# Kernel tuning notes

Hardware: AMD Instinct MI355X
Metric: run time of the kernel (lower is better)

The kernel has to match this reference:

```python
import jax, jax.numpy as jnp
import numpy as np

N_TYPES = 4  # global / and / or / leaf node types (indep_weights)


def gcn_layer(x, W_stack, b, edge_src, edge_dst, edge_w, labels, num_nodes):
    # Per-node-type dense projection: compute all 4 projections, then select by label.
    # all4: [4, N, out]
    all4 = jnp.einsum('nd,kdo->kno', x, W_stack)
    support = jnp.take_along_axis(all4, labels[None, :, None].astype(jnp.int32), axis=0)[0]  # [N, out]
    # Sparse adjacency propagation: out[dst] += w * support[src]  (torch.spmm equivalent)
    msgs = support[edge_src] * edge_w[:, None]  # [E, out]
    agg = jax.ops.segment_sum(msgs, edge_dst, num_segments=num_nodes)
    return agg + b


def setup_inputs() -> dict:
    key = jax.random.key(0)
    ks = jax.random.split(key, 12)
    N, E = 50000, 1600000
    nfeat, nhid, nclass = 256, 256, 64
    x = jax.random.normal(ks[0], (N, nfeat), dtype=jnp.float32)
    edge_src = jax.random.randint(ks[1], (E,), 0, N, dtype=jnp.int32)
    edge_dst = jax.random.randint(ks[2], (E,), 0, N, dtype=jnp.int32)
    edge_w = jax.random.uniform(ks[3], (E,), dtype=jnp.float32)
    labels = jax.random.randint(ks[4], (N,), 0, N_TYPES, dtype=jnp.int32)
    def winit(k, fi, fo):
        s = 1.0 / np.sqrt(fo)
        return jax.random.uniform(k, (N_TYPES, fi, fo), minval=-s, maxval=s, dtype=jnp.float32)
    def binit(k, fo):
        s = 1.0 / np.sqrt(fo)
        return jax.random.uniform(k, (fo,), minval=-s, maxval=s, dtype=jnp.float32)
    return {
        'x': x, 'edge_src': edge_src, 'edge_dst': edge_dst, 'edge_w': edge_w, 'labels': labels,
        'W1': winit(ks[5], nfeat, nhid), 'b1': binit(ks[6], nhid),
        'W2': winit(ks[7], nhid, nhid), 'b2': binit(ks[8], nhid),
        'W3': winit(ks[9], nhid, nclass), 'b3': binit(ks[10], nclass),
    }


def reference(x, edge_src, edge_dst, edge_w, labels, W1, b1, W2, b2, W3, b3):
    N = x.shape[0]
    h = jax.nn.relu(gcn_layer(x, W1, b1, edge_src, edge_dst, edge_w, labels, N))
    # F.dropout with p=0 (module default) is identity
    h = jax.nn.relu(gcn_layer(h, W2, b2, edge_src, edge_dst, edge_w, labels, N))
    out = gcn_layer(h, W3, b3, edge_src, edge_dst, edge_w, labels, N)
    return out
```

## Files before the change

### kernel.cpp

```cpp
#include <hip/hip_runtime.h>
#include <hip/hip_bf16.h>

#define NT 4
#define FEAT 256
#define OUT3 64

typedef __bf16 bf16x8 __attribute__((ext_vector_type(8)));
typedef float  f32x4  __attribute__((ext_vector_type(4)));

__device__ inline unsigned int f2bf_bits(float f) {
    __hip_bfloat16 h = __float2bfloat16(f);
    unsigned short u;
    __builtin_memcpy(&u, &h, 2);
    return (unsigned int)u;
}
__device__ inline float bfl(unsigned int u) { return __uint_as_float(u << 16); }
__device__ inline float bfh(unsigned int u) { return __uint_as_float(u & 0xffff0000u); }
__device__ __host__ inline int nat_of(int p) {
    int lo = p & 63;
    return (p & ~63) | (((lo & 3) << 4) | (lo >> 2));
}

__global__ __launch_bounds__(512) void pass_a(const int* __restrict__ dst,
                                              const int* __restrict__ labels,
                                              int* __restrict__ bcnt, int* __restrict__ lc,
                                              int E, int N) {
    __shared__ int h[256];
    __shared__ int lh[NT];
    int tid = threadIdx.x;
    if (tid < 256) h[tid] = 0;
    if (tid < NT) lh[tid] = 0;
    __syncthreads();
    int base = blockIdx.x * 4096;
#pragma unroll
    for (int k = 0; k < 8; ++k) {
        int e = base + k * 512 + tid;
        if (e < E) atomicAdd(&h[((unsigned)dst[e]) >> 8], 1);
    }
#pragma unroll
    for (int k = 0; k < 8; ++k) {
        int i = base + k * 512 + tid;
        if (i < N) atomicAdd(&lh[labels[i]], 1);
    }
    __syncthreads();
    if (tid < 256) { int v = h[tid]; if (v) atomicAdd(&bcnt[tid], v); }
    if (tid < NT) { int v = lh[tid]; if (v) atomicAdd(&lc[tid], v); }
}

__global__ __launch_bounds__(256) void scan_master(
    const int* __restrict__ bcnt, const int* __restrict__ lc,
    int* __restrict__ boff, int* __restrict__ gcur, int* __restrict__ rowoff,
    int* __restrict__ lstart, int NB, int N, int E) {
    __shared__ int s[256];
    int tid = threadIdx.x;
    int own = (tid < NB) ? bcnt[tid] : 0;
    s[tid] = own;
    __syncthreads();
    for (int d = 1; d < 256; d <<= 1) {
        int v = (tid >= d) ? s[tid - d] : 0;
        __syncthreads();
        s[tid] += v;
        __syncthreads();
    }
    int excl = s[tid] - own;
    if (tid < NB) { boff[tid] = excl; gcur[tid] = excl; }
    if (tid == 0) {
        boff[NB] = E; rowoff[N] = E;
        int run = 0;
        for (int l = 0; l < NT; ++l) {
            lstart[l] = run;
            run += (lc[l] + 63) & ~63;
        }
    }
}

__global__ void scatter_nodes(const int* __restrict__ labels, const int* __restrict__ lstart,
                              int* __restrict__ lcur, int* __restrict__ iperm, int N) {
    int n = blockIdx.x * 256 + threadIdx.x;
    int lab = (n < N) ? labels[n] : -1;
    int lane = threadIdx.x & 63;
    for (int l = 0; l < NT; ++l) {
        unsigned long long m = __ballot(lab == l);
        if (m == 0ull) continue;
        int leader = __builtin_ctzll(m);
        int base = 0;
        if (lane == leader) base = atomicAdd(&lcur[l], (int)__popcll(m));
        base = __shfl(base, leader, 64);
        if (lab == l) {
            int prefix = (int)__popcll(m & ((1ull << lane) - 1ull));
            iperm[n] = lstart[l] + base + prefix;
        }
    }
}

__global__ __launch_bounds__(512) void fuse_a(
    const int* __restrict__ src, const int* __restrict__ dst, const float* __restrict__ w,
    const int* __restrict__ iperm, int* __restrict__ gcur, uint2* __restrict__ earr, int E,
    const float* __restrict__ x, unsigned short* __restrict__ actLo,
    unsigned short* __restrict__ actHi, int total4,
    const float* __restrict__ W1, const float* __restrict__ W2, const float* __restrict__ W3,
    const float* __restrict__ b1, const float* __restrict__ b2,
    unsigned short* __restrict__ W1b, unsigned short* __restrict__ W2b,
    unsigned short* __restrict__ W3b, float* __restrict__ biasPerm,
    int nbEB, int nbX) {
    int tid = threadIdx.x;
    int blk = (int)blockIdx.x;
    if (blk < nbEB) {
        __shared__ int h[256];
        __shared__ int basearr[256];
        if (tid < 256) h[tid] = 0;
        __syncthreads();
        int base = blk * 4096;
        int b[8], rank[8], px[8]; float wv[8];
#pragma unroll
        for (int k = 0; k < 8; ++k) {
            int e = base + k * 512 + tid;
            if (e < E) {
                int d = dst[e];
                b[k] = ((unsigned)d) >> 8;
                px[k] = iperm[src[e]] | ((d & 255) << 16);
                wv[k] = w[e];
                rank[k] = atomicAdd(&h[b[k]], 1);
            } else b[k] = -1;
        }
        __syncthreads();
        if (tid < 256) { int c = h[tid]; basearr[tid] = c ? atomicAdd(&gcur[tid], c) : 0; }
        __syncthreads();
#pragma unroll
        for (int k = 0; k < 8; ++k) {
            if (b[k] >= 0) {
                int pos = basearr[b[k]] + rank[k];
                earr[pos] = make_uint2((unsigned)px[k], __float_as_uint(wv[k]));
            }
        }
    } else if (blk < nbEB + nbX) {
        int i = (blk - nbEB) * 512 + tid;
        if (i < total4) {
            float4 v = ((const float4*)x)[i];
            unsigned int lo = f2bf_bits(v.x) | (f2bf_bits(v.y) << 16);
            unsigned int hi = f2bf_bits(v.z) | (f2bf_bits(v.w) << 16);
            int slot = iperm[i >> 6];
            unsigned short* dp = ((i & 63) >= 32) ? actHi : actLo;
            ((uint2*)dp)[(size_t)slot * 32 + (i & 31)] = make_uint2(lo, hi);
        }
    } else {
        const int S = NT * FEAT * FEAT;
        const int S3 = NT * FEAT * OUT3;
        int idx = (blk - nbEB - nbX) * 512 + tid;
        if (idx < 2 * S + S3) {
            const float* W; unsigned short* D; int OUTF; int t; bool remap;
            if (idx < S)          { W = W1; D = W1b; OUTF = FEAT; t = idx;         remap = false; }
            else if (idx < 2 * S) { W = W2; D = W2b; OUTF = FEAT; t = idx - S;     remap = true; }
            else                  { W = W3; D = W3b; OUTF = OUT3; t = idx - 2 * S; remap = true; }
            int n = t % OUTF;
            int r = t / OUTF;
            int j = r & 7, q = (r >> 3) & 3, k0 = (r >> 5) & 7, lab = r >> 8;
            int k_slot = k0 * 32 + q * 8 + j;
            int k_src = remap ? nat_of(k_slot) : k_slot;
            float f = W[((size_t)(lab * FEAT + k_src)) * OUTF + n];
            D[(((size_t)lab * 8 + k0) * OUTF + n) * 32 + q * 8 + j] = (unsigned short)f2bf_bits(f);
        } else {
            int p2 = idx - (2 * S + S3);
            if (p2 < 256) biasPerm[p2] = b1[nat_of(p2)];
            else if (p2 < 512) biasPerm[p2] = b2[nat_of(p2 - 256)];
        }
    }
}

__device__ void bucket_sort_body(int b, const uint2* __restrict__ earr,
                                 const int* __restrict__ boff, int* __restrict__ rowoff,
                                 unsigned int* __restrict__ edata, int N) {
    int s = boff[b], e = boff[b + 1];
    __shared__ int cnt[256], off[256];
    int tid = threadIdx.x;
    cnt[tid] = 0;
    __syncthreads();
    for (int i = s + tid; i < e; i += 256) atomicAdd(&cnt[(earr[i].x >> 16) & 255], 1);
    __syncthreads();
    off[tid] = cnt[tid];
    __syncthreads();
    for (int d = 1; d < 256; d <<= 1) {
        int v = (tid >= d) ? off[tid - d] : 0;
        __syncthreads();
        off[tid] += v;
        __syncthreads();
    }
    int excl = off[tid] - cnt[tid];
    int node = b * 256 + tid;
    if (node < N) rowoff[node] = s + excl;
    off[tid] = excl;
    __syncthreads();
    for (int i = s + tid; i < e; i += 256) {
        uint2 r = earr[i];
        int d = (r.x >> 16) & 255;
        int k = atomicAdd(&off[d], 1);
        edata[s + k] = (f2bf_bits(__uint_as_float(r.y)) << 16) | (r.x & 0xffff);
    }
}

__device__ void proj256_body(int gb,
                             const unsigned short* __restrict__ actLo,
                             const unsigned short* __restrict__ actHi,
                             const unsigned short* __restrict__ Wswz,
                             const int* __restrict__ lstart,
                             unsigned short* __restrict__ supLo,
                             unsigned short* __restrict__ supHi) {
    int warp = threadIdx.x >> 6;
    int lane = threadIdx.x & 63;
    int m0 = gb * 64;
    int lab = (m0 >= lstart[1]) + (m0 >= lstart[2]) + (m0 >= lstart[3]);
    int q = lane >> 4, c = lane & 15;
    int n0 = warp * 64;

    const unsigned short* aLo = actLo + (size_t)(m0 + c) * 128 + q * 8;
    const unsigned short* aHi = actHi + (size_t)(m0 + c) * 128 + q * 8;
    const unsigned short* bb = Wswz + (size_t)lab * FEAT * 256 + (size_t)(n0 + c) * 32 + q * 8;

    f32x4 acc[4][4] = {};
#pragma unroll
    for (int k0 = 0; k0 < 8; ++k0) {
        const unsigned short* abase = (k0 < 4) ? aLo : aHi;
        int koff = (k0 & 3) * 32;
        bf16x8 a[4];
#pragma unroll
        for (int t = 0; t < 4; ++t) a[t] = *(const bf16x8*)(abase + (size_t)t * 2048 + koff);
        const unsigned short* bk = bb + (size_t)k0 * 32 * 256;
#pragma unroll
        for (int u = 0; u < 4; ++u) {
            bf16x8 bfrag = *(const bf16x8*)(bk + u * 512);
#pragma unroll
            for (int t = 0; t < 4; ++t)
                acc[t][u] = __builtin_amdgcn_mfma_f32_16x16x32_bf16(a[t], bfrag, acc[t][u], 0, 0, 0);
        }
    }
    uint2* ov = (uint2*)((n0 >= 128) ? supHi : supLo);
    int cix = ((n0 & 64) >> 2) + c;
#pragma unroll
    for (int t = 0; t < 4; ++t) {
#pragma unroll
        for (int r = 0; r < 4; ++r) {
            int row = m0 + t * 16 + q * 4 + r;
            unsigned int lo = f2bf_bits(acc[t][0][r]) | (f2bf_bits(acc[t][1][r]) << 16);
            unsigned int hi = f2bf_bits(acc[t][2][r]) | (f2bf_bits(acc[t][3][r]) << 16);
            ov[(size_t)row * 32 + cix] = make_uint2(lo, hi);
        }
    }
}

__global__ __launch_bounds__(256) void fuse_b(
    const uint2* __restrict__ earr, const int* __restrict__ boff,
    int* __restrict__ rowoff, unsigned int* __restrict__ edata, int N, int NB,
    const unsigned short* __restrict__ actLo, const unsigned short* __restrict__ actHi,
    const unsigned short* __restrict__ Wswz, const int* __restrict__ lstart,
    unsigned short* __restrict__ supLo, unsigned short* __restrict__ supHi) {
    int blk = (int)blockIdx.x;
    if (blk < NB) bucket_sort_body(blk, earr, boff, rowoff, edata, N);
    else proj256_body(blk - NB, actLo, actHi, Wswz, lstart, supLo, supHi);
}

__global__ __launch_bounds__(256) void proj256_kernel(
    const unsigned short* __restrict__ actLo, const unsigned short* __restrict__ actHi,
    const unsigned short* __restrict__ Wswz, const int* __restrict__ lstart,
    unsigned short* __restrict__ supLo, unsigned short* __restrict__ supHi) {
    proj256_body((int)blockIdx.x, actLo, actHi, Wswz, lstart, supLo, supHi);
}

__global__ __launch_bounds__(256) void proj64_kernel(
    const unsigned short* __restrict__ actLo, const unsigned short* __restrict__ actHi,
    const unsigned short* __restrict__ Wswz, const int* __restrict__ lstart,
    unsigned short* __restrict__ outp) {
    int warp = threadIdx.x >> 6;
    int lane = threadIdx.x & 63;
    int m0 = blockIdx.x * 64;
    int lab = (m0 >= lstart[1]) + (m0 >= lstart[2]) + (m0 >= lstart[3]);
    int q = lane >> 4, c = lane & 15;
    int mb = m0 + warp * 16;

    const unsigned short* aLo = actLo + (size_t)(mb + c) * 128 + q * 8;
    const unsigned short* aHi = actHi + (size_t)(mb + c) * 128 + q * 8;
    const unsigned short* bb = Wswz + (size_t)lab * FEAT * OUT3 + (size_t)c * 32 + q * 8;

    f32x4 acc[4] = {};
#pragma unroll
    for (int k0 = 0; k0 < 8; ++k0) {
        const unsigned short* abase = (k0 < 4) ? aLo : aHi;
        bf16x8 a = *(const bf16x8*)(abase + (k0 & 3) * 32);
        const unsigned short* bk = bb + (size_t)k0 * 32 * OUT3;
#pragma unroll
        for (int u = 0; u < 4; ++u) {
            bf16x8 bfrag = *(const bf16x8*)(bk + u * 512);
            acc[u] = __builtin_amdgcn_mfma_f32_16x16x32_bf16(a, bfrag, acc[u], 0, 0, 0);
        }
    }
    uint2* ov = (uint2*)outp;
#pragma unroll
    for (int r = 0; r < 4; ++r) {
        int row = mb + q * 4 + r;
        unsigned int lo = f2bf_bits(acc[0][r]) | (f2bf_bits(acc[1][r]) << 16);
        unsigned int hi = f2bf_bits(acc[2][r]) | (f2bf_bits(acc[3][r]) << 16);
        ov[(size_t)row * 16 + c] = make_uint2(lo, hi);
    }
}

__global__ __launch_bounds__(256) void agg256h_kernel(
    const unsigned int* __restrict__ sup, const int* __restrict__ rowoff,
    const unsigned int* __restrict__ edata, const int* __restrict__ iperm,
    const float* __restrict__ biasHalf, unsigned int* __restrict__ outp, int N) {
    int warp = __builtin_amdgcn_readfirstlane((int)(threadIdx.x >> 6));
    int node = (int)blockIdx.x * 4 + warp;
    if (node >= N) return;
    int lane = threadIdx.x & 63;
    int s = __builtin_amdgcn_readfirstlane(rowoff[node]);
    int e = __builtin_amdgcn_readfirstlane(rowoff[node + 1]);
    int slot = __builtin_amdgcn_readfirstlane(iperm[node]);
    float a0 = 0.f, a1 = 0.f;
    int j = s;
    for (; j + 16 <= e; j += 16) {
        unsigned int ed[16], v[16];
#pragma unroll
        for (int u = 0; u < 16; ++u) ed[u] = edata[j + u];
#pragma unroll
        for (int u = 0; u < 16; ++u) v[u] = sup[(size_t)(ed[u] & 0xffff) * 64 + lane];
#pragma unroll
        for (int u = 0; u < 16; ++u) {
            float w = __uint_as_float(ed[u] & 0xffff0000u);
            a0 += w * bfl(v[u]); a1 += w * bfh(v[u]);
        }
    }
    if (j < e) {
        unsigned int ed[16], v[16]; float wm[16];
#pragma unroll
        for (int u = 0; u < 16; ++u) {
            int jj = j + u;
            int jc = (jj < e) ? jj : e - 1;
            ed[u] = edata[jc];
            wm[u] = (jj < e) ? __uint_as_float(ed[u] & 0xffff0000u) : 0.f;
        }
#pragma unroll
        for (int u = 0; u < 16; ++u) v[u] = sup[(size_t)(ed[u] & 0xffff) * 64 + lane];
#pragma unroll
        for (int u = 0; u < 16; ++u) { a0 += wm[u] * bfl(v[u]); a1 += wm[u] * bfh(v[u]); }
    }
    float2 b = ((const float2*)biasHalf)[lane];
    a0 = fmaxf(a0 + b.x, 0.f);
    a1 = fmaxf(a1 + b.y, 0.f);
    outp[(size_t)slot * 64 + lane] = f2bf_bits(a0) | (f2bf_bits(a1) << 16);
}

__global__ __launch_bounds__(256) void agg64_kernel(
    const unsigned short* __restrict__ sup, const int* __restrict__ rowoff,
    const unsigned int* __restrict__ edata, const float* __restrict__ b3,
    float* __restrict__ outp, int N) {
    int warp = __builtin_amdgcn_readfirstlane((int)(threadIdx.x >> 6));
    int node = (int)blockIdx.x * 4 + warp;
    if (node >= N) return;
    int lane = threadIdx.x & 63;
    int s = __builtin_amdgcn_readfirstlane(rowoff[node]);
    int e = __builtin_amdgcn_readfirstlane(rowoff[node + 1]);
    float a = 0.f;
    int j = s;
    for (; j + 8 <= e; j += 8) {
        unsigned int ed[8]; unsigned short v[8];
#pragma unroll
        for (int u = 0; u < 8; ++u) ed[u] = edata[j + u];
#pragma unroll
        for (int u = 0; u < 8; ++u) v[u] = sup[(size_t)(ed[u] & 0xffff) * 64 + lane];
#pragma unroll
        for (int u = 0; u < 8; ++u)
            a += __uint_as_float(ed[u] & 0xffff0000u) * __uint_as_float((unsigned int)v[u] << 16);
    }
    if (j < e) {
        unsigned int ed[8]; float wm[8]; unsigned short v[8];
#pragma unroll
        for (int u = 0; u < 8; ++u) {
            int jj = j + u;
            int jc = (jj < e) ? jj : e - 1;
            ed[u] = edata[jc];
            wm[u] = (jj < e) ? __uint_as_float(ed[u] & 0xffff0000u) : 0.f;
        }
#pragma unroll
        for (int u = 0; u < 8; ++u) v[u] = sup[(size_t)(ed[u] & 0xffff) * 64 + lane];
#pragma unroll
        for (int u = 0; u < 8; ++u)
            a += wm[u] * __uint_as_float((unsigned int)v[u] << 16);
    }
    int natp = (((lane & 3) << 4) | (lane >> 2));
    outp[(size_t)node * 64 + natp] = a + b3[natp];
}

extern "C" void kernel_launch(void* const* d_in, const int* in_sizes, int n_in,
                              void* d_out, int out_size, void* d_ws, size_t ws_size,
                              hipStream_t stream) {
    const float* x        = (const float*)d_in[0];
    const int*   edge_src = (const int*)d_in[1];
    const int*   edge_dst = (const int*)d_in[2];
    const float* edge_w   = (const float*)d_in[3];
    const int*   labels   = (const int*)d_in[4];
    const float* W1 = (const float*)d_in[5];
    const float* b1 = (const float*)d_in[6];
    const float* W2 = (const float*)d_in[7];
    const float* b2 = (const float*)d_in[8];
    const float* W3 = (const float*)d_in[9];
    const float* b3 = (const float*)d_in[10];

    const int N = in_sizes[0] / FEAT;
    const int E = in_sizes[1];
    const int NB = (N + 255) >> 8;
    const int G64 = (N + NT * 64 + 63) / 64;
    const int slotCap = G64 * 64;

    char* p = (char*)d_ws;
    auto alloc = [&](size_t bytes) -> char* {
        char* r = p;
        p += (bytes + 255) & ~(size_t)255;
        return r;
    };
    unsigned short* bufA = (unsigned short*)alloc((size_t)slotCap * FEAT * 2);
    unsigned short* bufB = (unsigned short*)alloc((size_t)slotCap * FEAT * 2);
    unsigned short* W1b  = (unsigned short*)alloc((size_t)NT * FEAT * FEAT * 2);
    unsigned short* W2b  = (unsigned short*)alloc((size_t)NT * FEAT * FEAT * 2);
    unsigned short* W3b  = (unsigned short*)alloc((size_t)NT * FEAT * OUT3 * 2);
    float*        biasPerm = (float*)alloc(512 * 4);
    int*          rowoff = (int*)alloc((size_t)(N + 1) * 4);
    unsigned int* edata  = (unsigned int*)alloc((size_t)E * 4);
    int*          iperm  = (int*)alloc((size_t)N * 4);
    int*          counters = (int*)alloc(264 * 4);
    int*          boff   = (int*)alloc(257 * 4);
    int*          gcur   = (int*)alloc(256 * 4);
    int*          lstart = (int*)alloc(64);
    int* bcnt = counters;
    int* lc   = counters + 256;
    int* lcur = counters + 260;

    unsigned short* actLo = bufA;
    unsigned short* actHi = bufA + (size_t)slotCap * 128;
    unsigned short* supLo = bufB;
    unsigned short* supHi = bufB + (size_t)slotCap * 128;
    uint2* earr = (uint2*)d_out;

    const int nbEB = (E + 4095) / 4096;
    const int total4 = N * 64;
    const int nbX = (total4 + 511) / 512;
    const int totW = 2 * NT * FEAT * FEAT + NT * FEAT * OUT3 + 512;
    const int nbW = (totW + 511) / 512;

    hipMemsetAsync(counters, 0, 264 * 4, stream);
    pass_a<<<nbEB, 512, 0, stream>>>(edge_dst, labels, bcnt, lc, E, N);
    scan_master<<<1, 256, 0, stream>>>(bcnt, lc, boff, gcur, rowoff, lstart, NB, N, E);
    scatter_nodes<<<(N + 255) / 256, 256, 0, stream>>>(labels, lstart, lcur, iperm, N);
    fuse_a<<<nbEB + nbX + nbW, 512, 0, stream>>>(
        edge_src, edge_dst, edge_w, iperm, gcur, earr, E,
        x, actLo, actHi, total4,
        W1, W2, W3, b1, b2, W1b, W2b, W3b, biasPerm, nbEB, nbX);

    const int aggGrid = (N + 3) / 4;
    fuse_b<<<NB + G64, 256, 0, stream>>>(earr, boff, rowoff, edata, N, NB,
                                         actLo, actHi, W1b, lstart, supLo, supHi);
    agg256h_kernel<<<aggGrid, 256, 0, stream>>>((const unsigned int*)supLo, rowoff, edata, iperm,
                                                biasPerm + 0, (unsigned int*)actLo, N);
    agg256h_kernel<<<aggGrid, 256, 0, stream>>>((const unsigned int*)supHi, rowoff, edata, iperm,
                                                biasPerm + 128, (unsigned int*)actHi, N);
    proj256_kernel<<<G64, 256, 0, stream>>>(actLo, actHi, W2b, lstart, supLo, supHi);
    agg256h_kernel<<<aggGrid, 256, 0, stream>>>((const unsigned int*)supLo, rowoff, edata, iperm,
                                                biasPerm + 256, (unsigned int*)actLo, N);
    agg256h_kernel<<<aggGrid, 256, 0, stream>>>((const unsigned int*)supHi, rowoff, edata, iperm,
                                                biasPerm + 384, (unsigned int*)actHi, N);
    proj64_kernel<<<G64, 256, 0, stream>>>(actLo, actHi, W3b, lstart, bufB);
    agg64_kernel<<<aggGrid, 256, 0, stream>>>(bufB, rowoff, edata, b3, (float*)d_out, N);
}
```

Baseline: 481.2 us.

## Merge split Lo/Hi feature halves into single full-width rows and one aggregation pass

Activation and support buffers were stored as two 128-column halves, each aggregated by its own kernel launch. They become single 256-column bf16 rows. Each layer now runs one aggregation kernel that gathers 8 bytes per lane per edge, so edge metadata is read once instead of twice. The aggregation unroll drops from 16 to 8 edges, and outputs use nontemporal stores. The trade-off is a larger gather footprint per edge and fewer loads in flight, which may lower cache locality compared with the half-width passes.

```diff
diff --git a/kernel.cpp b/kernel.cpp
--- a/kernel.cpp
+++ b/kernel.cpp
@@ -7,6 +7,7 @@
 
 typedef __bf16 bf16x8 __attribute__((ext_vector_type(8)));
 typedef float  f32x4  __attribute__((ext_vector_type(4)));
+typedef unsigned int u32x2 __attribute__((ext_vector_type(2)));
 
 __device__ inline unsigned int f2bf_bits(float f) {
     __hip_bfloat16 h = __float2bfloat16(f);
@@ -96,8 +97,7 @@
 __global__ __launch_bounds__(512) void fuse_a(
     const int* __restrict__ src, const int* __restrict__ dst, const float* __restrict__ w,
     const int* __restrict__ iperm, int* __restrict__ gcur, uint2* __restrict__ earr, int E,
-    const float* __restrict__ x, unsigned short* __restrict__ actLo,
-    unsigned short* __restrict__ actHi, int total4,
+    const float* __restrict__ x, unsigned short* __restrict__ act, int total4,
     const float* __restrict__ W1, const float* __restrict__ W2, const float* __restrict__ W3,
     const float* __restrict__ b1, const float* __restrict__ b2,
     unsigned short* __restrict__ W1b, unsigned short* __restrict__ W2b,
@@ -140,8 +140,7 @@
             unsigned int lo = f2bf_bits(v.x) | (f2bf_bits(v.y) << 16);
             unsigned int hi = f2bf_bits(v.z) | (f2bf_bits(v.w) << 16);
             int slot = iperm[i >> 6];
-            unsigned short* dp = ((i & 63) >= 32) ? actHi : actLo;
-            ((uint2*)dp)[(size_t)slot * 32 + (i & 31)] = make_uint2(lo, hi);
+            ((uint2*)act)[(size_t)slot * 64 + (i & 63)] = make_uint2(lo, hi);
         }
     } else {
         const int S = NT * FEAT * FEAT;
@@ -199,12 +198,10 @@
 }
 
 __device__ void proj256_body(int gb,
-                             const unsigned short* __restrict__ actLo,
-                             const unsigned short* __restrict__ actHi,
+                             const unsigned short* __restrict__ act,
                              const unsigned short* __restrict__ Wswz,
                              const int* __restrict__ lstart,
-                             unsigned short* __restrict__ supLo,
-                             unsigned short* __restrict__ supHi) {
+                             unsigned short* __restrict__ sup) {
     int warp = threadIdx.x >> 6;
     int lane = threadIdx.x & 63;
     int m0 = gb * 64;
@@ -212,18 +209,16 @@
     int q = lane >> 4, c = lane & 15;
     int n0 = warp * 64;
 
-    const unsigned short* aLo = actLo + (size_t)(m0 + c) * 128 + q * 8;
-    const unsigned short* aHi = actHi + (size_t)(m0 + c) * 128 + q * 8;
+    const unsigned short* arow = act + (size_t)(m0 + c) * 256 + q * 8;
     const unsigned short* bb = Wswz + (size_t)lab * FEAT * 256 + (size_t)(n0 + c) * 32 + q * 8;
 
     f32x4 acc[4][4] = {};
 #pragma unroll
     for (int k0 = 0; k0 < 8; ++k0) {
-        const unsigned short* abase = (k0 < 4) ? aLo : aHi;
-        int koff = (k0 & 3) * 32;
+        const unsigned short* abase = arow + ((k0 & 3) * 32) + ((k0 < 4) ? 0 : 128);
         bf16x8 a[4];
 #pragma unroll
-        for (int t = 0; t < 4; ++t) a[t] = *(const bf16x8*)(abase + (size_t)t * 2048 + koff);
+        for (int t = 0; t < 4; ++t) a[t] = *(const bf16x8*)(abase + (size_t)t * 4096);
         const unsigned short* bk = bb + (size_t)k0 * 32 * 256;
 #pragma unroll
         for (int u = 0; u < 4; ++u) {
@@ -233,8 +228,8 @@
                 acc[t][u] = __builtin_amdgcn_mfma_f32_16x16x32_bf16(a[t], bfrag, acc[t][u], 0, 0, 0);
         }
     }
-    uint2* ov = (uint2*)((n0 >= 128) ? supHi : supLo);
-    int cix = ((n0 & 64) >> 2) + c;
+    uint2* ov = (uint2*)sup;
+    int cix = (n0 >> 2) + c;
 #pragma unroll
     for (int t = 0; t < 4; ++t) {
 #pragma unroll
@@ -242,7 +237,7 @@
             int row = m0 + t * 16 + q * 4 + r;
             unsigned int lo = f2bf_bits(acc[t][0][r]) | (f2bf_bits(acc[t][1][r]) << 16);
             unsigned int hi = f2bf_bits(acc[t][2][r]) | (f2bf_bits(acc[t][3][r]) << 16);
-            ov[(size_t)row * 32 + cix] = make_uint2(lo, hi);
+            ov[(size_t)row * 64 + cix] = make_uint2(lo, hi);
         }
     }
 }
@@ -250,23 +245,23 @@
 __global__ __launch_bounds__(256) void fuse_b(
     const uint2* __restrict__ earr, const int* __restrict__ boff,
     int* __restrict__ rowoff, unsigned int* __restrict__ edata, int N, int NB,
-    const unsigned short* __restrict__ actLo, const unsigned short* __restrict__ actHi,
+    const unsigned short* __restrict__ act,
     const unsigned short* __restrict__ Wswz, const int* __restrict__ lstart,
-    unsigned short* __restrict__ supLo, unsigned short* __restrict__ supHi) {
+    unsigned short* __restrict__ sup) {
     int blk = (int)blockIdx.x;
     if (blk < NB) bucket_sort_body(blk, earr, boff, rowoff, edata, N);
-    else proj256_body(blk - NB, actLo, actHi, Wswz, lstart, supLo, supHi);
+    else proj256_body(blk - NB, act, Wswz, lstart, sup);
 }
 
 __global__ __launch_bounds__(256) void proj256_kernel(
-    const unsigned short* __restrict__ actLo, const unsigned short* __restrict__ actHi,
+    const unsigned short* __restrict__ act,
     const unsigned short* __restrict__ Wswz, const int* __restrict__ lstart,
-    unsigned short* __restrict__ supLo, unsigned short* __restrict__ supHi) {
-    proj256_body((int)blockIdx.x, actLo, actHi, Wswz, lstart, supLo, supHi);
+    unsigned short* __restrict__ sup) {
+    proj256_body((int)blockIdx.x, act, Wswz, lstart, sup);
 }
 
 __global__ __launch_bounds__(256) void proj64_kernel(
-    const unsigned short* __restrict__ actLo, const unsigned short* __restrict__ actHi,
+    const unsigned short* __restrict__ act,
     const unsigned short* __restrict__ Wswz, const int* __restrict__ lstart,
     unsigned short* __restrict__ outp) {
     int warp = threadIdx.x >> 6;
@@ -276,15 +271,13 @@
     int q = lane >> 4, c = lane & 15;
     int mb = m0 + warp * 16;
 
-    const unsigned short* aLo = actLo + (size_t)(mb + c) * 128 + q * 8;
-    const unsigned short* aHi = actHi + (size_t)(mb + c) * 128 + q * 8;
+    const unsigned short* arow = act + (size_t)(mb + c) * 256 + q * 8;
     const unsigned short* bb = Wswz + (size_t)lab * FEAT * OUT3 + (size_t)c * 32 + q * 8;
 
     f32x4 acc[4] = {};
 #pragma unroll
     for (int k0 = 0; k0 < 8; ++k0) {
-        const unsigned short* abase = (k0 < 4) ? aLo : aHi;
-        bf16x8 a = *(const bf16x8*)(abase + (k0 & 3) * 32);
+        bf16x8 a = *(const bf16x8*)(arow + ((k0 & 3) * 32) + ((k0 < 4) ? 0 : 128));
         const unsigned short* bk = bb + (size_t)k0 * 32 * OUT3;
 #pragma unroll
         for (int u = 0; u < 4; ++u) {
@@ -302,10 +295,10 @@
     }
 }
 
-__global__ __launch_bounds__(256) void agg256h_kernel(
-    const unsigned int* __restrict__ sup, const int* __restrict__ rowoff,
+__global__ __launch_bounds__(256) void agg256_kernel(
+    const uint2* __restrict__ sup, const int* __restrict__ rowoff,
     const unsigned int* __restrict__ edata, const int* __restrict__ iperm,
-    const float* __restrict__ biasHalf, unsigned int* __restrict__ outp, int N) {
+    const float* __restrict__ bias, u32x2* __restrict__ outp, int N) {
     int warp = __builtin_amdgcn_readfirstlane((int)(threadIdx.x >> 6));
     int node = (int)blockIdx.x * 4 + warp;
     if (node >= N) return;
@@ -313,38 +306,47 @@
     int s = __builtin_amdgcn_readfirstlane(rowoff[node]);
     int e = __builtin_amdgcn_readfirstlane(rowoff[node + 1]);
     int slot = __builtin_amdgcn_readfirstlane(iperm[node]);
-    float a0 = 0.f, a1 = 0.f;
+    float a0 = 0.f, a1 = 0.f, a2 = 0.f, a3 = 0.f;
     int j = s;
-    for (; j + 16 <= e; j += 16) {
-        unsigned int ed[16], v[16];
-#pragma unroll
-        for (int u = 0; u < 16; ++u) ed[u] = edata[j + u];
-#pragma unroll
-        for (int u = 0; u < 16; ++u) v[u] = sup[(size_t)(ed[u] & 0xffff) * 64 + lane];
-#pragma unroll
-        for (int u = 0; u < 16; ++u) {
+    for (; j + 8 <= e; j += 8) {
+        unsigned int ed[8]; uint2 v[8];
+#pragma unroll
+        for (int u = 0; u < 8; ++u) ed[u] = edata[j + u];
+#pragma unroll
+        for (int u = 0; u < 8; ++u) v[u] = sup[(size_t)(ed[u] & 0xffff) * 64 + lane];
+#pragma unroll
+        for (int u = 0; u < 8; ++u) {
             float w = __uint_as_float(ed[u] & 0xffff0000u);
-            a0 += w * bfl(v[u]); a1 += w * bfh(v[u]);
+            a0 += w * bfl(v[u].x); a1 += w * bfh(v[u].x);
+            a2 += w * bfl(v[u].y); a3 += w * bfh(v[u].y);
         }
     }
     if (j < e) {
-        unsigned int ed[16], v[16]; float wm[16];
-#pragma unroll
-        for (int u = 0; u < 16; ++u) {
+        unsigned int ed[8]; uint2 v[8]; float wm[8];
+#pragma unroll
+        for (int u = 0; u < 8; ++u) {
             int jj = j + u;
             int jc = (jj < e) ? jj : e - 1;
             ed[u] = edata[jc];
             wm[u] = (jj < e) ? __uint_as_float(ed[u] & 0xffff0000u) : 0.f;
         }
 #pragma unroll
-        for (int u = 0; u < 16; ++u) v[u] = sup[(size_t)(ed[u] & 0xffff) * 64 + lane];
-#pragma unroll
-        for (int u = 0; u < 16; ++u) { a0 += wm[u] * bfl(v[u]); a1 += wm[u] * bfh(v[u]); }
-    }
-    float2 b = ((const float2*)biasHalf)[lane];
+        for (int u = 0; u < 8; ++u) v[u] = sup[(size_t)(ed[u] & 0xffff) * 64 + lane];
+#pragma unroll
+        for (int u = 0; u < 8; ++u) {
+            a0 += wm[u] * bfl(v[u].x); a1 += wm[u] * bfh(v[u].x);
+            a2 += wm[u] * bfl(v[u].y); a3 += wm[u] * bfh(v[u].y);
+        }
+    }
+    float4 b = ((const float4*)bias)[lane];
     a0 = fmaxf(a0 + b.x, 0.f);
     a1 = fmaxf(a1 + b.y, 0.f);
-    outp[(size_t)slot * 64 + lane] = f2bf_bits(a0) | (f2bf_bits(a1) << 16);
+    a2 = fmaxf(a2 + b.z, 0.f);
+    a3 = fmaxf(a3 + b.w, 0.f);
+    u32x2 o;
+    o[0] = f2bf_bits(a0) | (f2bf_bits(a1) << 16);
+    o[1] = f2bf_bits(a2) | (f2bf_bits(a3) << 16);
+    __builtin_nontemporal_store(o, &outp[(size_t)slot * 64 + lane]);
 }
 
 __global__ __launch_bounds__(256) void agg64_kernel(
@@ -432,10 +434,8 @@
     int* lc   = counters + 256;
     int* lcur = counters + 260;
 
-    unsigned short* actLo = bufA;
-    unsigned short* actHi = bufA + (size_t)slotCap * 128;
-    unsigned short* supLo = bufB;
-    unsigned short* supHi = bufB + (size_t)slotCap * 128;
+    unsigned short* act = bufA;
+    unsigned short* sup = bufB;
     uint2* earr = (uint2*)d_out;
 
     const int nbEB = (E + 4095) / 4096;
@@ -450,21 +450,17 @@
     scatter_nodes<<<(N + 255) / 256, 256, 0, stream>>>(labels, lstart, lcur, iperm, N);
     fuse_a<<<nbEB + nbX + nbW, 512, 0, stream>>>(
         edge_src, edge_dst, edge_w, iperm, gcur, earr, E,
-        x, actLo, actHi, total4,
+        x, act, total4,
         W1, W2, W3, b1, b2, W1b, W2b, W3b, biasPerm, nbEB, nbX);
 
     const int aggGrid = (N + 3) / 4;
     fuse_b<<<NB + G64, 256, 0, stream>>>(earr, boff, rowoff, edata, N, NB,
-                                         actLo, actHi, W1b, lstart, supLo, supHi);
-    agg256h_kernel<<<aggGrid, 256, 0, stream>>>((const unsigned int*)supLo, rowoff, edata, iperm,
-                                                biasPerm + 0, (unsigned int*)actLo, N);
-    agg256h_kernel<<<aggGrid, 256, 0, stream>>>((const unsigned int*)supHi, rowoff, edata, iperm,
-                                                biasPerm + 128, (unsigned int*)actHi, N);
-    proj256_kernel<<<G64, 256, 0, stream>>>(actLo, actHi, W2b, lstart, supLo, supHi);
-    agg256h_kernel<<<aggGrid, 256, 0, stream>>>((const unsigned int*)supLo, rowoff, edata, iperm,
-                                                biasPerm + 256, (unsigned int*)actLo, N);
-    agg256h_kernel<<<aggGrid, 256, 0, stream>>>((const unsigned int*)supHi, rowoff, edata, iperm,
-                                                biasPerm + 384, (unsigned int*)actHi, N);
-    proj64_kernel<<<G64, 256, 0, stream>>>(actLo, actHi, W3b, lstart, bufB);
+                                         act, W1b, lstart, sup);
+    agg256_kernel<<<aggGrid, 256, 0, stream>>>((const uint2*)sup, rowoff, edata, iperm,
+                                               biasPerm + 0, (u32x2*)act, N);
+    proj256_kernel<<<G64, 256, 0, stream>>>(act, W2b, lstart, sup);
+    agg256_kernel<<<aggGrid, 256, 0, stream>>>((const uint2*)sup, rowoff, edata, iperm,
+                                               biasPerm + 256, (u32x2*)act, N);
+    proj64_kernel<<<G64, 256, 0, stream>>>(act, W3b, lstart, bufB);
     agg64_kernel<<<aggGrid, 256, 0, stream>>>(bufB, rowoff, edata, b3, (float*)d_out, N);
 }
```

After: 492.1 us. +2.3%, slower.
